# Optimization experiments

Measured on AMD Instinct MI355X. Metric: run time of the kernel, lower is better.

Reference implementation:

```python
import jax, jax.numpy as jnp
import numpy as np

E = 8          # num_experts
D = 512        # embed_dim
FF = 4         # ff_mult
H = D * FF     # hidden
B, N = 4, 2048
TOP_K = 2


def setup_inputs() -> dict:
    key = jax.random.key(0)
    ks = jax.random.split(key, 6)
    tokens = jax.random.normal(ks[0], (B, N, D), dtype=jnp.float32)
    # token-choice top-k routing: logits -> top-2 experts per token
    logits = jax.random.normal(ks[1], (B, N, E), dtype=jnp.float32)
    topv, topi = jax.lax.top_k(logits, TOP_K)            # (B,N,K)
    disp = jnp.zeros((B, N, E), jnp.float32)
    disp = jnp.take_along_axis(disp, topi, axis=-1)  # placeholder shape trick avoided below
    disp = jnp.zeros((B, N, E), jnp.float32).at[
        jnp.arange(B)[:, None, None], jnp.arange(N)[None, :, None], topi
    ].set(1.0)                                            # (B,N,E) 0/1 dispatch mask
    w = jax.nn.softmax(topv, axis=-1)                     # combine weights over selected
    comb = jnp.zeros((B, N, E), jnp.float32).at[
        jnp.arange(B)[:, None, None], jnp.arange(N)[None, :, None], topi
    ].set(w)
    # expert params (xavier-ish scale); out_proj gain 0.02 as in module init
    Wg = jax.random.normal(ks[2], (E, D, H), dtype=jnp.float32) * (2.0 / (D + H)) ** 0.5
    Wv = jax.random.normal(ks[3], (E, D, H), dtype=jnp.float32) * (2.0 / (D + H)) ** 0.5
    Wo = jax.random.normal(ks[4], (E, H, D), dtype=jnp.float32) * 0.02 * (2.0 / (D + H)) ** 0.5
    scales = jnp.full((E,), 1.0 / E, dtype=jnp.float32)   # output_scale per expert
    return {"tokens": tokens, "dispatch_weights": disp, "combine_weights": comb,
            "Wg": Wg, "Wv": Wv, "Wo": Wo, "scales": scales}


def reference(tokens, dispatch_weights, combine_weights, Wg, Wv, Wo, scales):
    """ExpertPool.forward: per-expert SwiGLU FFN, combined by routing weights.

    Dense-masked formulation (same math as gather->FFN->weighted scatter-add:
    expert outputs only contribute where dispatch>0).
    """
    b, n, d = tokens.shape
    x = tokens.reshape(b * n, d)                          # (M, D)
    gate = jax.nn.gelu(jnp.einsum('md,edh->emh', x, Wg), approximate=False)
    value = jnp.einsum('md,edh->emh', x, Wv)
    out_e = jnp.einsum('emh,ehd->emd', gate * value, Wo) * scales[:, None, None]
    mask = dispatch_weights.reshape(b * n, -1) > 0        # (M, E)
    w = jnp.where(mask, combine_weights.reshape(b * n, -1), 0.0)
    out = jnp.einsum('emd,me->md', out_e, w)              # weighted combine
    return out.reshape(b, n, d)
```

## Files before the change

### kernel.cpp

```cpp
#include <hip/hip_runtime.h>
#include <hip/hip_bf16.h>


#define NEXP 8
#define DIM 512
#define HID 2048
#define MTOK 8192
#define PMAX (2*MTOK)
#define TM 128
#define MT 144

typedef __bf16 bf16;
typedef __bf16 bf16x8 __attribute__((ext_vector_type(8)));
typedef float  f32x4  __attribute__((ext_vector_type(4)));

#define WAITVM(N) asm volatile("s_waitcnt vmcnt(" #N ")" ::: "memory")
#define SCHED0    __builtin_amdgcn_sched_barrier(0)
#define BAR       __builtin_amdgcn_s_barrier

__device__ __forceinline__ void gload16(const bf16* g, bf16* l) {
  __builtin_amdgcn_global_load_lds(
      (const __attribute__((address_space(1))) void*)g,
      (__attribute__((address_space(3))) void*)l, 16, 0, 0);
}

__global__ __launch_bounds__(256) void k_cvt_x(const float* __restrict__ in,
                                               bf16* __restrict__ out, int n4) {
  int i = blockIdx.x*256 + threadIdx.x;
  if (i >= n4) return;
  float4 v = ((const float4* __restrict__)in)[i];
  bf16 o[4];
  o[0]=(bf16)v.x; o[1]=(bf16)v.y; o[2]=(bf16)v.z; o[3]=(bf16)v.w;
  *(uint2*)&out[(size_t)i*4] = *(uint2*)o;
}

__global__ __launch_bounds__(256) void k_tcvt2(const float* __restrict__ in0,
                                               const float* __restrict__ in1,
                                               bf16* __restrict__ out0,
                                               bf16* __restrict__ out1, int R, int C) {
  __shared__ __align__(16) bf16 t[64][72];
  const int z = blockIdx.z;
  const int e = z & (NEXP-1);
  const float* __restrict__ pin = ((z < NEXP) ? in0 : in1) + (size_t)e*R*C;
  bf16* __restrict__ pout = ((z < NEXP) ? out0 : out1) + (size_t)e*R*C;
  const int c0 = blockIdx.x*64, r0 = blockIdx.y*64;
  const int tid = threadIdx.x;
  const int rr = tid>>4, cc4 = (tid&15)*4;
#pragma unroll
  for (int i=0;i<4;i++){
    int r = i*16 + rr;
    float4 v = *(const float4*)&pin[(size_t)(r0+r)*C + c0 + cc4];
    t[cc4+0][r]=(bf16)v.x; t[cc4+1][r]=(bf16)v.y;
    t[cc4+2][r]=(bf16)v.z; t[cc4+3][r]=(bf16)v.w;
  }
  __syncthreads();
#pragma unroll
  for (int i=0;i<4;i++){
    int c = i*16 + rr;
    *(uint2*)&pout[(size_t)(c0+c)*R + r0 + cc4] = *(uint2*)&t[c][cc4];
  }
}

__global__ __launch_bounds__(256) void k_count(const float* __restrict__ disp,
                                               int* __restrict__ cnt) {
  __shared__ int lc[NEXP];
  int t = threadIdx.x;
  if (t < NEXP) lc[t] = 0;
  __syncthreads();
  int m = blockIdx.x*256 + t;
  float4 d0 = *(const float4*)&disp[(size_t)m*NEXP];
  float4 d1 = *(const float4*)&disp[(size_t)m*NEXP+4];
  if (d0.x>0.f) atomicAdd(&lc[0],1);
  if (d0.y>0.f) atomicAdd(&lc[1],1);
  if (d0.z>0.f) atomicAdd(&lc[2],1);
  if (d0.w>0.f) atomicAdd(&lc[3],1);
  if (d1.x>0.f) atomicAdd(&lc[4],1);
  if (d1.y>0.f) atomicAdd(&lc[5],1);
  if (d1.z>0.f) atomicAdd(&lc[6],1);
  if (d1.w>0.f) atomicAdd(&lc[7],1);
  __syncthreads();
  if (t < NEXP) atomicAdd(&cnt[t], lc[t]);
}

__global__ void k_scan(const int* __restrict__ cnt, int* __restrict__ base,
                       int* __restrict__ te, int* __restrict__ trow, int* __restrict__ tn) {
  __shared__ int sb[NEXP+1], st[NEXP+1], sc[NEXP];
  if (threadIdx.x == 0){
    int b=0, t=0;
    for (int e=0;e<NEXP;e++){
      sb[e]=b; st[e]=t; sc[e]=cnt[e]; base[e]=b;
      b += sc[e];
      t += (sc[e]+TM-1)/TM;
    }
    sb[NEXP]=b; st[NEXP]=t;
  }
  __syncthreads();
  for (int idx=threadIdx.x; idx<MT; idx+=blockDim.x){
    int e=-1;
#pragma unroll
    for (int q=0;q<NEXP;q++) if (idx>=st[q] && idx<st[q+1]) e=q;
    if (e>=0){
      int k = idx - st[e];
      int nr = sc[e] - k*TM; if (nr>TM) nr=TM;
      te[idx]=e; trow[idx]=sb[e]+k*TM; tn[idx]=nr;
    } else te[idx]=-1;
  }
}

__global__ __launch_bounds__(256) void k_fill(const float* __restrict__ disp,
    const float* __restrict__ comb, const float* __restrict__ scales,
    const int* __restrict__ base, int* __restrict__ fillc,
    int* __restrict__ stok, float* __restrict__ sw, int* __restrict__ sslot) {
  int m = blockIdx.x*256 + threadIdx.x;
  int jj = 0;
#pragma unroll
  for (int e=0;e<NEXP;e++){
    float dv = disp[(size_t)m*NEXP + e];
    if (dv > 0.f) {
      int s = atomicAdd(&fillc[e], 1);
      int g = base[e] + s;
      stok[g] = m;
      sw[g] = comb[(size_t)m*NEXP + e] * scales[e];
      if (jj < 2) sslot[m*2 + jj] = g;
      jj++;
    }
  }
}

__global__ __launch_bounds__(256) void k_gemm1(const bf16* __restrict__ Xb,
    const bf16* __restrict__ WgT, const bf16* __restrict__ WvT,
    const int* __restrict__ te, const int* __restrict__ trow, const int* __restrict__ tn,
    const int* __restrict__ stok, bf16* __restrict__ H1) {
  const int tile = blockIdx.y;
  const int e = te[tile];
  if (e < 0) return;
  const int row0 = trow[tile], nrows = tn[tile];
  const int n0 = blockIdx.x*64;
  __shared__ __align__(16) bf16 Al[2*TM*64];
  __shared__ __align__(16) bf16 Bgl[2*64*64];
  __shared__ __align__(16) bf16 Bvl[2*64*64];
  const int tid = threadIdx.x, lane = tid&63;
  const int wr = (tid>>7)&1, wc = (tid>>6)&1;
  const bf16* __restrict__ wg = WgT + (size_t)e*HID*DIM;
  const bf16* __restrict__ wv = WvT + (size_t)e*HID*DIM;

  const bf16* asrc[4];
#pragma unroll
  for (int i=0;i<4;i++){
    int c = i*256 + tid;
    int r = c>>3, qs = (c&7) ^ (r&7);
    int gr = (r < nrows) ? (row0 + r) : row0;
    asrc[i] = Xb + (size_t)stok[gr]*DIM + qs*8;
  }
  const bf16 *bsg[2], *bsv[2];
#pragma unroll
  for (int j=0;j<2;j++){
    int c = j*256 + tid;
    int r = c>>3, qs = (c&7) ^ (r&7);
    size_t o = (size_t)(n0 + r)*DIM + qs*8;
    bsg[j] = wg + o; bsv[j] = wv + o;
  }
  const int wbase = (tid&192)*8;

  auto stage = [&](int bi, int kt){
    const int k0 = kt*64;
#pragma unroll
    for (int i=0;i<4;i++)
      gload16(asrc[i]+k0, Al + bi*TM*64 + i*2048 + wbase);
#pragma unroll
    for (int j=0;j<2;j++){
      gload16(bsg[j]+k0, Bgl + bi*64*64 + j*2048 + wbase);
      gload16(bsv[j]+k0, Bvl + bi*64*64 + j*2048 + wbase);
    }
  };

  f32x4 accg[4][2] = {}, accv[4][2] = {};
  const int rsw = (lane&7)<<3;
  stage(0, 0);
  for (int kt=0; kt<DIM/64; ++kt){
    const int bi = kt&1;
    if (kt+1 < DIM/64){ stage(bi^1, kt+1); WAITVM(8); }
    else WAITVM(0);
    BAR(); SCHED0;
#pragma unroll
    for (int ks=0; ks<2; ks++){
      const int kos = (ks*32 + (lane>>4)*8) ^ rsw;
      bf16x8 a[4], bg[2], bv[2];
#pragma unroll
      for (int ni=0; ni<2; ni++){
        bg[ni] = *(const bf16x8*)&Bgl[bi*4096 + (wc*32 + ni*16 + (lane&15))*64 + kos];
        bv[ni] = *(const bf16x8*)&Bvl[bi*4096 + (wc*32 + ni*16 + (lane&15))*64 + kos];
      }
#pragma unroll
      for (int mi=0; mi<4; mi++)
        a[mi] = *(const bf16x8*)&Al[bi*TM*64 + (wr*64 + mi*16 + (lane&15))*64 + kos];
#pragma unroll
      for (int mi=0; mi<4; mi++)
#pragma unroll
        for (int ni=0; ni<2; ni++){
          accg[mi][ni] = __builtin_amdgcn_mfma_f32_16x16x32_bf16(a[mi], bg[ni], accg[mi][ni], 0,0,0);
          accv[mi][ni] = __builtin_amdgcn_mfma_f32_16x16x32_bf16(a[mi], bv[ni], accv[mi][ni], 0,0,0);
        }
    }
    BAR(); SCHED0;
  }
  const int cb = n0 + wc*32 + (lane&15);
  const int rb = wr*64 + (lane>>4)*4;
#pragma unroll
  for (int mi=0; mi<4; mi++)
#pragma unroll
    for (int j=0; j<4; j++){
      int r = rb + mi*16 + j;
      if (r < nrows){
#pragma unroll
        for (int ni=0; ni<2; ni++){
          float g = accg[mi][ni][j], v = accv[mi][ni][j];
          float ge = 0.5f*g*(1.f + erff(g*0.70710678118654752f));
          H1[(size_t)(row0+r)*HID + cb + ni*16] = (bf16)(ge*v);
        }
      }
    }
}

__global__ __launch_bounds__(256) void k_gemm2(const bf16* __restrict__ H1,
    const bf16* __restrict__ WoT,
    const int* __restrict__ te, const int* __restrict__ trow, const int* __restrict__ tn,
    const float* __restrict__ sw, float* __restrict__ gout) {
  const int tile = blockIdx.y;
  const int e = te[tile];
  if (e < 0) return;
  const int row0 = trow[tile], nrows = tn[tile];
  const int n0 = blockIdx.x*128;
  __shared__ __align__(16) bf16 Al[2*TM*64];
  __shared__ __align__(16) bf16 Bl[2*TM*64];
  const int tid = threadIdx.x, lane = tid&63;
  const int wr = (tid>>7)&1, wc = (tid>>6)&1;
  const bf16* __restrict__ wo = WoT + (size_t)e*DIM*HID;

  const bf16 *asrc[4], *bsrc[4];
#pragma unroll
  for (int i=0;i<4;i++){
    int c = i*256 + tid;
    int r = c>>3, qs = (c&7) ^ (r&7);
    int ar = (r < nrows) ? (row0 + r) : row0;
    asrc[i] = H1 + (size_t)ar*HID + qs*8;
    bsrc[i] = wo + (size_t)(n0 + r)*HID + qs*8;
  }
  const int wbase = (tid&192)*8;

  auto stage = [&](int bi, int kt){
    const int k0 = kt*64;
#pragma unroll
    for (int i=0;i<4;i++){
      gload16(asrc[i]+k0, Al + bi*TM*64 + i*2048 + wbase);
      gload16(bsrc[i]+k0, Bl + bi*TM*64 + i*2048 + wbase);
    }
  };

  f32x4 acc[4][4] = {};
  const int rsw = (lane&7)<<3;
  stage(0, 0);
  for (int kt=0; kt<HID/64; ++kt){
    const int bi = kt&1;
    if (kt+1 < HID/64){ stage(bi^1, kt+1); WAITVM(8); }
    else WAITVM(0);
    BAR(); SCHED0;
#pragma unroll
    for (int ks=0; ks<2; ks++){
      const int kos = (ks*32 + (lane>>4)*8) ^ rsw;
      bf16x8 a[4], b[4];
#pragma unroll
      for (int ni=0; ni<4; ni++)
        b[ni] = *(const bf16x8*)&Bl[bi*TM*64 + (wc*64 + ni*16 + (lane&15))*64 + kos];
#pragma unroll
      for (int mi=0; mi<4; mi++)
        a[mi] = *(const bf16x8*)&Al[bi*TM*64 + (wr*64 + mi*16 + (lane&15))*64 + kos];
#pragma unroll
      for (int mi=0; mi<4; mi++)
#pragma unroll
        for (int ni=0; ni<4; ni++)
          acc[mi][ni] = __builtin_amdgcn_mfma_f32_16x16x32_bf16(a[mi], b[ni], acc[mi][ni], 0,0,0);
    }
    BAR(); SCHED0;
  }
  const int cb = n0 + wc*64 + (lane&15);
  const int rb = wr*64 + (lane>>4)*4;
#pragma unroll
  for (int mi=0; mi<4; mi++)
#pragma unroll
    for (int j=0; j<4; j++){
      int r = rb + mi*16 + j;
      if (r < nrows){
        int slot = row0 + r;
        float wgt = sw[slot];
        float* op = gout + (size_t)slot*DIM + cb;
#pragma unroll
        for (int ni=0; ni<4; ni++)
          op[ni*16] = acc[mi][ni][j] * wgt;
      }
    }
}

__global__ __launch_bounds__(256) void k_comb(const float* __restrict__ gout,
    const int* __restrict__ sslot, float* __restrict__ out) {
  int idx = blockIdx.x*256 + threadIdx.x;
  int m = idx >> 7, c4 = (idx & 127)*4;
  int s0 = sslot[m*2], s1 = sslot[m*2+1];
  float4 x = *(const float4*)&gout[(size_t)s0*DIM + c4];
  float4 y = *(const float4*)&gout[(size_t)s1*DIM + c4];
  x.x += y.x; x.y += y.y; x.z += y.z; x.w += y.w;
  *(float4*)&out[(size_t)m*DIM + c4] = x;
}

extern "C" void kernel_launch(void* const* d_in, const int* in_sizes, int n_in,
                              void* d_out, int out_size, void* d_ws, size_t ws_size,
                              hipStream_t stream) {
  const float* tokens = (const float*)d_in[0];
  const float* disp   = (const float*)d_in[1];
  const float* comb   = (const float*)d_in[2];
  const float* Wg     = (const float*)d_in[3];
  const float* Wv     = (const float*)d_in[4];
  const float* Wo     = (const float*)d_in[5];
  const float* scales = (const float*)d_in[6];
  float* out = (float*)d_out;

  size_t off = 0;
  char* wsb = (char*)d_ws;
  auto take = [&](size_t bytes)->char* {
    char* q = wsb + off; off += (bytes + 255) & ~(size_t)255; return q;
  };
  int*   cnt   = (int*)  take(NEXP*4);
  int*   basee = (int*)  take(NEXP*4);
  int*   fillc = (int*)  take(NEXP*4);
  int*   te    = (int*)  take(MT*4);
  int*   trow  = (int*)  take(MT*4);
  int*   tnr   = (int*)  take(MT*4);
  int*   stok  = (int*)  take((size_t)PMAX*4);
  float* sw    = (float*)take((size_t)PMAX*4);
  int*   sslot = (int*)  take((size_t)MTOK*2*4);
  bf16*  Xb    = (bf16*) take((size_t)MTOK*DIM*2);
  bf16*  WgT   = (bf16*) take((size_t)NEXP*DIM*HID*2);
  bf16*  WvT   = (bf16*) take((size_t)NEXP*DIM*HID*2);
  bf16*  WoT   = (bf16*) take((size_t)NEXP*DIM*HID*2);
  bf16*  H1    = (bf16*) take((size_t)PMAX*HID*2);
  float* gout  = (float*)WgT;
  (void)ws_size; (void)in_sizes; (void)n_in; (void)out_size;

  hipMemsetAsync(d_ws, 0, 768, stream);

  k_cvt_x<<<dim3((MTOK*DIM/4)/256), 256, 0, stream>>>(tokens, Xb, MTOK*DIM/4);
  k_tcvt2<<<dim3(HID/64, DIM/64, 2*NEXP), 256, 0, stream>>>(Wg, Wv, WgT, WvT, DIM, HID);
  k_tcvt2<<<dim3(DIM/64, HID/64, NEXP), 256, 0, stream>>>(Wo, Wo, WoT, WoT, HID, DIM);
  k_count<<<dim3(MTOK/256), 256, 0, stream>>>(disp, cnt);
  k_scan <<<1, 64, 0, stream>>>(cnt, basee, te, trow, tnr);
  k_fill <<<dim3(MTOK/256), 256, 0, stream>>>(disp, comb, scales, basee, fillc, stok, sw, sslot);
  k_gemm1<<<dim3(HID/64, MT), 256, 0, stream>>>(Xb, WgT, WvT, te, trow, tnr, stok, H1);
  k_gemm2<<<dim3(DIM/128, MT), 256, 0, stream>>>(H1, WoT, te, trow, tnr, sw, gout);
  k_comb <<<dim3(MTOK*DIM/4/256), 256, 0, stream>>>(gout, sslot, out);
}
```

Measured before the change: 249.3 us.

## Halve gemm1 K-tile to 32 and remap gemm2 blocks across XCDs

The gate/value GEMM now stages K in 32-wide slices instead of 64, which halves its LDS footprint and changes the swizzle to match the narrower rows. The intent is higher occupancy, at the cost of twice as many barriers and pipeline stages. The down-projection GEMM switches to a 1D grid whose block-to-tile mapping groups tiles of the same expert onto the same XCD (the L&7 term), for better L2 reuse of that expert's weights. The mapping hardcodes 8 XCDs and 144 tiles (8*18).

```diff
diff --git a/kernel.cpp b/kernel.cpp
--- a/kernel.cpp
+++ b/kernel.cpp
@@ -136,75 +136,66 @@
   if (e < 0) return;
   const int row0 = trow[tile], nrows = tn[tile];
   const int n0 = blockIdx.x*64;
-  __shared__ __align__(16) bf16 Al[2*TM*64];
-  __shared__ __align__(16) bf16 Bgl[2*64*64];
-  __shared__ __align__(16) bf16 Bvl[2*64*64];
+  __shared__ __align__(16) bf16 Al[2*128*32];
+  __shared__ __align__(16) bf16 Bgl[2*64*32];
+  __shared__ __align__(16) bf16 Bvl[2*64*32];
   const int tid = threadIdx.x, lane = tid&63;
   const int wr = (tid>>7)&1, wc = (tid>>6)&1;
   const bf16* __restrict__ wg = WgT + (size_t)e*HID*DIM;
   const bf16* __restrict__ wv = WvT + (size_t)e*HID*DIM;
 
-  const bf16* asrc[4];
-#pragma unroll
-  for (int i=0;i<4;i++){
+  const bf16* asrc[2];
+#pragma unroll
+  for (int i=0;i<2;i++){
     int c = i*256 + tid;
-    int r = c>>3, qs = (c&7) ^ (r&7);
+    int r = c>>2, qs = (c&3) ^ ((r>>1)&3);
     int gr = (r < nrows) ? (row0 + r) : row0;
     asrc[i] = Xb + (size_t)stok[gr]*DIM + qs*8;
   }
-  const bf16 *bsg[2], *bsv[2];
-#pragma unroll
-  for (int j=0;j<2;j++){
-    int c = j*256 + tid;
-    int r = c>>3, qs = (c&7) ^ (r&7);
+  const bf16 *bsg, *bsv;
+  {
+    int r = tid>>2, qs = (tid&3) ^ ((r>>1)&3);
     size_t o = (size_t)(n0 + r)*DIM + qs*8;
-    bsg[j] = wg + o; bsv[j] = wv + o;
+    bsg = wg + o; bsv = wv + o;
   }
   const int wbase = (tid&192)*8;
 
   auto stage = [&](int bi, int kt){
-    const int k0 = kt*64;
-#pragma unroll
-    for (int i=0;i<4;i++)
-      gload16(asrc[i]+k0, Al + bi*TM*64 + i*2048 + wbase);
-#pragma unroll
-    for (int j=0;j<2;j++){
-      gload16(bsg[j]+k0, Bgl + bi*64*64 + j*2048 + wbase);
-      gload16(bsv[j]+k0, Bvl + bi*64*64 + j*2048 + wbase);
-    }
+    const int k0 = kt*32;
+    gload16(asrc[0]+k0, Al + bi*4096 + wbase);
+    gload16(asrc[1]+k0, Al + bi*4096 + 2048 + wbase);
+    gload16(bsg+k0, Bgl + bi*2048 + wbase);
+    gload16(bsv+k0, Bvl + bi*2048 + wbase);
   };
 
   f32x4 accg[4][2] = {}, accv[4][2] = {};
-  const int rsw = (lane&7)<<3;
+  const int r15 = lane&15;
+  const int koff = ((lane>>4) ^ ((r15>>1)&3))*8;
   stage(0, 0);
-  for (int kt=0; kt<DIM/64; ++kt){
+  for (int kt=0; kt<DIM/32; ++kt){
     const int bi = kt&1;
-    if (kt+1 < DIM/64){ stage(bi^1, kt+1); WAITVM(8); }
+    if (kt+1 < DIM/32){ stage(bi^1, kt+1); WAITVM(4); }
     else WAITVM(0);
     BAR(); SCHED0;
-#pragma unroll
-    for (int ks=0; ks<2; ks++){
-      const int kos = (ks*32 + (lane>>4)*8) ^ rsw;
-      bf16x8 a[4], bg[2], bv[2];
+    bf16x8 a[4], bg[2], bv[2];
+#pragma unroll
+    for (int ni=0; ni<2; ni++){
+      bg[ni] = *(const bf16x8*)&Bgl[bi*2048 + (wc*32 + ni*16 + r15)*32 + koff];
+      bv[ni] = *(const bf16x8*)&Bvl[bi*2048 + (wc*32 + ni*16 + r15)*32 + koff];
+    }
+#pragma unroll
+    for (int mi=0; mi<4; mi++)
+      a[mi] = *(const bf16x8*)&Al[bi*4096 + (wr*64 + mi*16 + r15)*32 + koff];
+#pragma unroll
+    for (int mi=0; mi<4; mi++)
 #pragma unroll
       for (int ni=0; ni<2; ni++){
-        bg[ni] = *(const bf16x8*)&Bgl[bi*4096 + (wc*32 + ni*16 + (lane&15))*64 + kos];
-        bv[ni] = *(const bf16x8*)&Bvl[bi*4096 + (wc*32 + ni*16 + (lane&15))*64 + kos];
+        accg[mi][ni] = __builtin_amdgcn_mfma_f32_16x16x32_bf16(a[mi], bg[ni], accg[mi][ni], 0,0,0);
+        accv[mi][ni] = __builtin_amdgcn_mfma_f32_16x16x32_bf16(a[mi], bv[ni], accv[mi][ni], 0,0,0);
       }
-#pragma unroll
-      for (int mi=0; mi<4; mi++)
-        a[mi] = *(const bf16x8*)&Al[bi*TM*64 + (wr*64 + mi*16 + (lane&15))*64 + kos];
-#pragma unroll
-      for (int mi=0; mi<4; mi++)
-#pragma unroll
-        for (int ni=0; ni<2; ni++){
-          accg[mi][ni] = __builtin_amdgcn_mfma_f32_16x16x32_bf16(a[mi], bg[ni], accg[mi][ni], 0,0,0);
-          accv[mi][ni] = __builtin_amdgcn_mfma_f32_16x16x32_bf16(a[mi], bv[ni], accv[mi][ni], 0,0,0);
-        }
-    }
     BAR(); SCHED0;
   }
-  const int cb = n0 + wc*32 + (lane&15);
+  const int cb = n0 + wc*32 + r15;
   const int rb = wr*64 + (lane>>4)*4;
 #pragma unroll
   for (int mi=0; mi<4; mi++)
@@ -226,11 +217,12 @@
     const bf16* __restrict__ WoT,
     const int* __restrict__ te, const int* __restrict__ trow, const int* __restrict__ tn,
     const float* __restrict__ sw, float* __restrict__ gout) {
-  const int tile = blockIdx.y;
+  const int L = blockIdx.x;
+  const int tile = (L&7)*18 + (L>>5);
+  const int n0 = ((L>>3)&3)*128;
   const int e = te[tile];
   if (e < 0) return;
   const int row0 = trow[tile], nrows = tn[tile];
-  const int n0 = blockIdx.x*128;
   __shared__ __align__(16) bf16 Al[2*TM*64];
   __shared__ __align__(16) bf16 Bl[2*TM*64];
   const int tid = threadIdx.x, lane = tid&63;
@@ -355,6 +347,6 @@
   k_scan <<<1, 64, 0, stream>>>(cnt, basee, te, trow, tnr);
   k_fill <<<dim3(MTOK/256), 256, 0, stream>>>(disp, comb, scales, basee, fillc, stok, sw, sslot);
   k_gemm1<<<dim3(HID/64, MT), 256, 0, stream>>>(Xb, WgT, WvT, te, trow, tnr, stok, H1);
-  k_gemm2<<<dim3(DIM/128, MT), 256, 0, stream>>>(H1, WoT, te, trow, tnr, sw, gout);
+  k_gemm2<<<dim3(8*18*4), 256, 0, stream>>>(H1, WoT, te, trow, tnr, sw, gout);
   k_comb <<<dim3(MTOK*DIM/4/256), 256, 0, stream>>>(gout, sslot, out);
 }
```

Result: faster. 229.7 us (-7.8%).
